# Kernel optimization log

Hardware: AMD Instinct MI355X
Metric: run time of the kernel (lower is better)

Reference implementation:

```python
import jax, jax.numpy as jnp
import numpy as np

B, T, D, H = 4, 2048, 1024, 16
Hd = D // H


def setup_inputs() -> dict:
    key = jax.random.key(0)
    ks = jax.random.split(key, 6)
    s = 1.0 / np.sqrt(D)
    return {
        "x": jax.random.normal(ks[0], (B, T, D), dtype=jnp.float32),
        "mask": jnp.zeros((B, T), dtype=bool),
        "Wq": jax.random.normal(ks[1], (D, D), dtype=jnp.float32) * s,
        "bq": jnp.zeros((D,), dtype=jnp.float32),
        "Wk": jax.random.normal(ks[2], (D, D), dtype=jnp.float32) * s,
        "bk": jnp.zeros((D,), dtype=jnp.float32),
        "Wv": jax.random.normal(ks[3], (D, D), dtype=jnp.float32) * s,
        "bv": jnp.zeros((D,), dtype=jnp.float32),
        "Wo": jax.random.normal(ks[4], (D, D), dtype=jnp.float32) * s,
        "bo": jnp.zeros((D,), dtype=jnp.float32),
    }


def reference(x, mask, Wq, bq, Wk, bk, Wv, bv, Wo, bo):
    b, t, d = x.shape
    # projections -> [B, T, H, Hd]
    Q = (x @ Wq + bq).reshape(b, t, H, Hd)
    K = (x @ Wk + bk).reshape(b, t, H, Hd)
    V = (x @ Wv + bv).reshape(b, t, H, Hd)
    scale = jnp.asarray(Hd, x.dtype) ** -0.5
    # full score matrix [B, H, Tq, Tk] (matches the naive torch impl)
    attn = jnp.einsum("bqhd,bkhd->bhqk", Q, K) * scale
    attn = jnp.where(mask[:, None, None, :], jnp.asarray(-1e9, attn.dtype), attn)
    attn = jax.nn.softmax(attn, axis=-1)
    out = jnp.einsum("bhqk,bkhd->bqhd", attn, V).reshape(b, t, d)
    return out @ Wo + bo
```

## Files before the change

kernel.cpp:

```cpp
#include <hip/hip_runtime.h>

using bf16 = __bf16;
typedef bf16 bf16x4 __attribute__((ext_vector_type(4)));
typedef bf16 bf16x8 __attribute__((ext_vector_type(8)));
typedef float f32x4 __attribute__((ext_vector_type(4)));
typedef float f32x8 __attribute__((ext_vector_type(8)));

#define MFMA16(a, b, c) __builtin_amdgcn_mfma_f32_16x16x32_bf16(a, b, c, 0, 0, 0)

constexpr int Bb = 4, Tt = 2048, Dd = 1024, Hh = 16, Hd = 64;
constexpr int Mrows = Bb * Tt;
constexpr float CEXP = 0.18033688011112042f;

__device__ __forceinline__ void gload_lds16(const bf16* g, bf16* lds_base) {
  __builtin_amdgcn_global_load_lds((const __attribute__((address_space(1))) void*)g,
                                   (__attribute__((address_space(3))) void*)lds_base,
                                   16, 0, 0);
}

__global__ void cast_f32_bf16_kernel(const float* __restrict__ in, bf16* __restrict__ out) {
  size_t i = ((size_t)blockIdx.x * 256 + threadIdx.x) * 8;
  f32x8 v = *(const f32x8*)(in + i);
  *(bf16x8*)(out + i) = __builtin_convertvector(v, bf16x8);
}

__global__ void transpose_cast_w4_kernel(const float* __restrict__ Wq, const float* __restrict__ Wk,
                                         const float* __restrict__ Wv, const float* __restrict__ Wo,
                                         bf16* __restrict__ Wt, bf16* __restrict__ Wot) {
  __shared__ alignas(16) float tile[64][68];
  const int tid = threadIdx.x;
  const int n0 = blockIdx.x * 64, k0 = blockIdx.y * 64, z = blockIdx.z;
  const float* W = (z == 0) ? Wq : (z == 1) ? Wk : (z == 2) ? Wv : Wo;
  bf16* dst = (z == 3) ? Wot : (Wt + (size_t)z * Dd * Dd);
  const float scale = (z == 0) ? CEXP : 1.0f;
#pragma unroll
  for (int it = 0; it < 4; ++it) {
    int chunk = tid + it * 256;
    int kr = chunk >> 4, c4 = chunk & 15;
    f32x4 v = *(const f32x4*)(W + (size_t)(k0 + kr) * Dd + n0 + c4 * 4);
    *(f32x4*)&tile[kr][c4 * 4] = v * scale;
  }
  __syncthreads();
#pragma unroll
  for (int it = 0; it < 2; ++it) {
    int chunk = tid + it * 256;
    int n = chunk & 63, k8 = chunk >> 6;
    bf16x8 o;
#pragma unroll
    for (int j = 0; j < 8; ++j) o[j] = (bf16)tile[k8 * 8 + j][n];
    *(bf16x8*)(dst + (size_t)(n0 + n) * Dd + k0 + k8 * 8) = o;
  }
}

__global__ void pack_bias_kernel(const float* __restrict__ bq, const float* __restrict__ bk,
                                 const float* __restrict__ bv, float* __restrict__ outb) {
  int i = blockIdx.x * 256 + threadIdx.x;
  float v = (i < 1024) ? bq[i] * CEXP : (i < 2048 ? bk[i - 1024] : bv[i - 2048]);
  outb[i] = v;
}

constexpr int QBM = 256, QBN = 256, QBK = 32, QNT = Dd / QBK;

#define VMW(n) asm volatile("s_waitcnt vmcnt(" #n ")" ::: "memory")

__global__ __launch_bounds__(512, 2)
void gemm_qkv_kernel(const bf16* __restrict__ A, const bf16* __restrict__ Bt,
                     const float* __restrict__ bias, bf16* __restrict__ QK,
                     bf16* __restrict__ Vt) {
  constexpr int KD = Dd;
  __shared__ alignas(16) bf16 As[4][QBM * QBK];
  __shared__ alignas(16) bf16 Bs[4][QBN * QBK];
  const int tid = threadIdx.x;
  const int lane = tid & 63, wave = tid >> 6;
  const int col = lane & 15, quad = lane >> 4;
  const int wr = wave >> 2, wc = wave & 3;
  const size_t m0 = (size_t)blockIdx.x * QBM, n0 = (size_t)blockIdx.y * QBN;

  const int u = (lane & 7) ^ (lane >> 3);
  const int srow = 2 * (lane >> 3) + (u >> 2);
  const int scol = (u & 3) * 8;
  const bf16* Abase = A + (m0 + srow) * (size_t)KD + scol;
  const bf16* Bbase = Bt + (n0 + srow) * (size_t)KD + scol;

  const int pswz = (((col & 1) << 2) | quad) ^ (col >> 1);
  const int afb = wr * 4096 + (col >> 1) * 64 + pswz * 8;
  const int bfb = wc * 2048 + (col >> 1) * 64 + pswz * 8;

  f32x4 acc[8][4];
#pragma unroll
  for (int i = 0; i < 8; ++i)
#pragma unroll
    for (int j = 0; j < 4; ++j)
#pragma unroll
      for (int r = 0; r < 4; ++r) acc[i][j][r] = 0.f;

#define QSTAGE_A(t, sl) do { \
    gload_lds16(Abase + (size_t)(t) * QBK + (size_t)(2 * wave + 0) * 16 * KD, &As[sl][(2 * wave + 0) * 512]); \
    gload_lds16(Abase + (size_t)(t) * QBK + (size_t)(2 * wave + 1) * 16 * KD, &As[sl][(2 * wave + 1) * 512]); \
  } while (0)
#define QSTAGE_B(t, sl) do { \
    gload_lds16(Bbase + (size_t)(t) * QBK + (size_t)(2 * wave + 0) * 16 * KD, &Bs[sl][(2 * wave + 0) * 512]); \
    gload_lds16(Bbase + (size_t)(t) * QBK + (size_t)(2 * wave + 1) * 16 * KD, &Bs[sl][(2 * wave + 1) * 512]); \
  } while (0)

#define QKV_TILE(sl, STAGE0, STAGE1, VM) do { \
    bf16x8 af[4], bfv[4]; \
    _Pragma("unroll") for (int j = 0; j < 4; ++j) bfv[j] = *(const bf16x8*)&Bs[sl][bfb + j * 512]; \
    _Pragma("unroll") for (int i = 0; i < 4; ++i) af[i] = *(const bf16x8*)&As[sl][afb + i * 512]; \
    STAGE0; \
    __builtin_amdgcn_s_barrier(); \
    asm volatile("s_waitcnt lgkmcnt(0)" ::: "memory"); \
    __builtin_amdgcn_s_setprio(1); \
    _Pragma("unroll") for (int i = 0; i < 4; ++i) \
      _Pragma("unroll") for (int j = 0; j < 4; ++j) acc[i][j] = MFMA16(af[i], bfv[j], acc[i][j]); \
    __builtin_amdgcn_s_setprio(0); \
    __builtin_amdgcn_s_barrier(); \
    _Pragma("unroll") for (int i = 0; i < 4; ++i) af[i] = *(const bf16x8*)&As[sl][afb + (4 + i) * 512]; \
    STAGE1; \
    __builtin_amdgcn_s_barrier(); \
    asm volatile("s_waitcnt lgkmcnt(0)" ::: "memory"); \
    __builtin_amdgcn_s_setprio(1); \
    _Pragma("unroll") for (int i = 0; i < 4; ++i) \
      _Pragma("unroll") for (int j = 0; j < 4; ++j) acc[4 + i][j] = MFMA16(af[i], bfv[j], acc[4 + i][j]); \
    __builtin_amdgcn_s_setprio(0); \
    VM; \
    __builtin_amdgcn_s_barrier(); \
  } while (0)

  QSTAGE_A(0, 0); QSTAGE_B(0, 0);
  QSTAGE_A(1, 1); QSTAGE_B(1, 1);
  QSTAGE_A(2, 2); QSTAGE_B(2, 2);
  VMW(8);
  __builtin_amdgcn_s_barrier();

#pragma unroll 1
  for (int t = 0; t < QNT - 4; t += 4) {
    QKV_TILE(0, QSTAGE_A(t + 3, 3), QSTAGE_B(t + 3, 3), VMW(8));
    QKV_TILE(1, QSTAGE_A(t + 4, 0), QSTAGE_B(t + 4, 0), VMW(8));
    QKV_TILE(2, QSTAGE_A(t + 5, 1), QSTAGE_B(t + 5, 1), VMW(8));
    QKV_TILE(3, QSTAGE_A(t + 6, 2), QSTAGE_B(t + 6, 2), VMW(8));
  }
  QKV_TILE(0, QSTAGE_A(31, 3), QSTAGE_B(31, 3), VMW(8));
  QKV_TILE(1, (void)0, (void)0, VMW(4));
  QKV_TILE(2, (void)0, (void)0, VMW(0));
  QKV_TILE(3, (void)0, (void)0, (void)0);

  if (n0 < 2048) {
#pragma unroll
    for (int i = 0; i < 8; ++i)
#pragma unroll
      for (int j = 0; j < 4; ++j) {
        size_t row = m0 + wr * 128 + i * 16 + quad * 4;
        size_t c = n0 + wc * 64 + j * 16 + col;
        float bv = bias[c];
#pragma unroll
        for (int r = 0; r < 4; ++r) QK[(row + r) * 2048 + c] = (bf16)(acc[i][j][r] + bv);
      }
  } else {
#pragma unroll
    for (int i = 0; i < 8; ++i)
#pragma unroll
      for (int j = 0; j < 4; ++j) {
        size_t row = m0 + wr * 128 + i * 16 + quad * 4;
        int c = (int)(n0 + wc * 64 + j * 16 + col);
        float bv = bias[c];
        int dall = c - 2048, hh = dall >> 6, dd = dall & 63;
        int bi = (int)(row >> 11), trow = (int)(row & 2047);
        bf16x4 pk;
#pragma unroll
        for (int r = 0; r < 4; ++r) pk[r] = (bf16)(acc[i][j][r] + bv);
        *(bf16x4*)&Vt[((size_t)(bi * Hh + hh) * Hd + dd) * Tt + trow] = pk;
      }
  }
#undef QKV_TILE
#undef QSTAGE_A
#undef QSTAGE_B
}

__global__ __launch_bounds__(256)
void gemm_bf16_kernel(const bf16* __restrict__ A, const bf16* __restrict__ Bt,
                      const float* __restrict__ bias, float* __restrict__ C,
                      int M, int N, int K) {
  __shared__ alignas(16) bf16 As[128 * 64];
  __shared__ alignas(16) bf16 Bs[128 * 64];
  const int tid = threadIdx.x;
  const int lane = tid & 63, wave = tid >> 6;
  const int col = lane & 15, quad = lane >> 4;
  const int wr = (wave >> 1) * 64, wc = (wave & 1) * 64;
  const size_t m0 = (size_t)blockIdx.x * 128, n0 = (size_t)blockIdx.y * 128;
  const int srow = lane >> 3, schunk = (lane & 7) * 8;

  f32x4 acc[4][4];
#pragma unroll
  for (int i = 0; i < 4; ++i)
#pragma unroll
    for (int j = 0; j < 4; ++j)
#pragma unroll
      for (int r = 0; r < 4; ++r) acc[i][j][r] = 0.f;

  for (int k0 = 0; k0 < K; k0 += 64) {
#pragma unroll
    for (int it = 0; it < 4; ++it) {
      int rbase = it * 32 + wave * 8;
      gload_lds16(A + (m0 + rbase + srow) * (size_t)K + k0 + schunk, &As[rbase * 64]);
      gload_lds16(Bt + (n0 + rbase + srow) * (size_t)K + k0 + schunk, &Bs[rbase * 64]);
    }
    __syncthreads();
#pragma unroll
    for (int kk = 0; kk < 2; ++kk) {
      bf16x8 af[4], bfr[4];
#pragma unroll
      for (int i = 0; i < 4; ++i) af[i] = *(const bf16x8*)&As[(wr + i * 16 + col) * 64 + kk * 32 + quad * 8];
#pragma unroll
      for (int j = 0; j < 4; ++j) bfr[j] = *(const bf16x8*)&Bs[(wc + j * 16 + col) * 64 + kk * 32 + quad * 8];
#pragma unroll
      for (int i = 0; i < 4; ++i)
#pragma unroll
        for (int j = 0; j < 4; ++j) acc[i][j] = MFMA16(af[i], bfr[j], acc[i][j]);
    }
    __syncthreads();
  }
#pragma unroll
  for (int i = 0; i < 4; ++i)
#pragma unroll
    for (int j = 0; j < 4; ++j) {
      size_t row = m0 + wr + i * 16 + quad * 4;
      size_t c = n0 + wc + j * 16 + col;
      float bv = bias[c];
#pragma unroll
      for (int r = 0; r < 4; ++r) C[(row + r) * (size_t)N + c] = acc[i][j][r] + bv;
    }
}

__global__ __launch_bounds__(256, 2)
void flash_attn_kernel(const bf16* __restrict__ qk, const bf16* __restrict__ vt,
                       const unsigned char* __restrict__ mask, bf16* __restrict__ ao) {
  __shared__ alignas(16) bf16 Ks[2][64 * 64];
  __shared__ alignas(16) bf16 Vs[2][64 * 64];

  const int tid = threadIdx.x;
  const int wave = tid >> 6, lane = tid & 63;
  const int col = lane & 15, quad = lane >> 4;
  const int id = blockIdx.x;
  const int hb = id & 63, qi = id >> 6;
  const int h = hb & 15, b = hb >> 4;
  const int qbase0 = qi * 128 + wave * 32;

  const bf16* Qp = qk + (size_t)(b * Tt) * 2048 + h * Hd;
  const bf16* Kp = Qp + 1024;
  const bf16* Vp = vt + ((size_t)(b * Hh + h) * Hd) * Tt;
  const unsigned char* mp = mask + b * Tt;

  unsigned long long anym;
  {
    const unsigned long long* mq = (const unsigned long long*)mp;
    unsigned long long acc = 0;
#pragma unroll
    for (int j = 0; j < 4; ++j) acc |= mq[lane * 4 + j];
    anym = __ballot(acc != 0ull);
  }

  bf16x8 qf[2][2];
#pragma unroll
  for (int t = 0; t < 2; ++t)
#pragma unroll
    for (int kk = 0; kk < 2; ++kk)
      qf[t][kk] = *(const bf16x8*)(Qp + (size_t)(qbase0 + t * 16 + col) * 2048 + kk * 32 + quad * 8);

  const int u = (lane & 7) ^ (lane >> 3);
  const int g0 = 2 * wave, g1 = 2 * wave + 1;
  const bf16* Ksrc0 = Kp + (size_t)(g0 * 8 + (lane >> 3)) * 2048 + u * 8;
  const bf16* Ksrc1 = Kp + (size_t)(g1 * 8 + (lane >> 3)) * 2048 + u * 8;
  const bf16* Vsrc0 = Vp + (size_t)(g0 * 8 + (lane >> 3)) * 2048 + u * 8;
  const bf16* Vsrc1 = Vp + (size_t)(g1 * 8 + (lane >> 3)) * 2048 + u * 8;

  gload_lds16(Ksrc0, &Ks[0][g0 * 512]);
  gload_lds16(Ksrc1, &Ks[0][g1 * 512]);
  gload_lds16(Vsrc0, &Vs[0][g0 * 512]);
  gload_lds16(Vsrc1, &Vs[0][g1 * 512]);
  __syncthreads();

  f32x4 oacc[2][4];
  f32x4 lones[2];
#pragma unroll
  for (int t = 0; t < 2; ++t) {
#pragma unroll
    for (int r = 0; r < 4; ++r) lones[t][r] = 0.f;
#pragma unroll
    for (int n = 0; n < 4; ++n)
#pragma unroll
      for (int r = 0; r < 4; ++r) oacc[t][n][r] = 0.f;
  }
  const f32x4 zero4 = {0.f, 0.f, 0.f, 0.f};
  bf16x8 onev;
#pragma unroll
  for (int j = 0; j < 8; ++j) onev[j] = (bf16)1.0f;

  const int fslot0 = ((0 * 4 + quad) ^ (col & 7)) * 8;
  const int fslot1 = ((1 * 4 + quad) ^ (col & 7)) * 8;
  const int voff = (quad & 1) * 4;

  for (int i = 0; i < 32; ++i) {
    const int cur = i & 1, nxt = cur ^ 1;
    const int kb = i * 64;

    if (i < 31) {
      gload_lds16(Ksrc0 + (size_t)(kb + 64) * 2048, &Ks[nxt][g0 * 512]);
      gload_lds16(Ksrc1 + (size_t)(kb + 64) * 2048, &Ks[nxt][g1 * 512]);
      gload_lds16(Vsrc0 + (kb + 64), &Vs[nxt][g0 * 512]);
      gload_lds16(Vsrc1 + (kb + 64), &Vs[nxt][g1 * 512]);
    }

    bf16x8 kf[4][2], vfs[4][2];
#pragma unroll
    for (int kt = 0; kt < 4; ++kt) {
      kf[kt][0] = *(const bf16x8*)&Ks[cur][(kt * 16 + col) * 64 + fslot0];
      kf[kt][1] = *(const bf16x8*)&Ks[cur][(kt * 16 + col) * 64 + fslot1];
    }
#pragma unroll
    for (int n = 0; n < 4; ++n) {
      const int row = (n * 16 + col) * 64;
      const int rx = col & 7;
#pragma unroll
      for (int kk = 0; kk < 2; ++kk) {
        bf16x4 lo = *(const bf16x4*)&Vs[cur][row + ((kk * 4 + 0 + (quad >> 1)) ^ rx) * 8 + voff];
        bf16x4 hi = *(const bf16x4*)&Vs[cur][row + ((kk * 4 + 2 + (quad >> 1)) ^ rx) * 8 + voff];
        vfs[n][kk] = __builtin_shufflevector(lo, hi, 0, 1, 2, 3, 4, 5, 6, 7);
      }
    }

#pragma unroll
    for (int t = 0; t < 2; ++t) {
      f32x4 s[4];
#pragma unroll
      for (int kt = 0; kt < 4; ++kt) s[kt] = MFMA16(kf[kt][0], qf[t][0], zero4);
#pragma unroll
      for (int kt = 0; kt < 4; ++kt) s[kt] = MFMA16(kf[kt][1], qf[t][1], s[kt]);

      if ((anym >> (2 * i)) & 3ull) {
#pragma unroll
        for (int kt = 0; kt < 4; ++kt)
#pragma unroll
          for (int r = 0; r < 4; ++r)
            if (mp[kb + kt * 16 + quad * 4 + r] != 0) s[kt][r] = -1e9f;
      }

      f32x4 e[4];
#pragma unroll
      for (int kt = 0; kt < 4; ++kt)
#pragma unroll
        for (int r = 0; r < 4; ++r) e[kt][r] = __builtin_amdgcn_exp2f(s[kt][r]);
      bf16x4 c0 = __builtin_convertvector(e[0], bf16x4);
      bf16x4 c1 = __builtin_convertvector(e[1], bf16x4);
      bf16x4 c2 = __builtin_convertvector(e[2], bf16x4);
      bf16x4 c3 = __builtin_convertvector(e[3], bf16x4);
      bf16x8 pf0 = __builtin_shufflevector(c0, c1, 0, 1, 2, 3, 4, 5, 6, 7);
      bf16x8 pf1 = __builtin_shufflevector(c2, c3, 0, 1, 2, 3, 4, 5, 6, 7);
#pragma unroll
      for (int n = 0; n < 4; ++n) {
        oacc[t][n] = MFMA16(pf0, vfs[n][0], oacc[t][n]);
        oacc[t][n] = MFMA16(pf1, vfs[n][1], oacc[t][n]);
      }
      lones[t] = MFMA16(pf0, onev, lones[t]);
      lones[t] = MFMA16(pf1, onev, lones[t]);
    }

    __syncthreads();
  }

#pragma unroll
  for (int t = 0; t < 2; ++t) {
    f32x4 rl;
#pragma unroll
    for (int r = 0; r < 4; ++r) rl[r] = __builtin_amdgcn_rcpf(lones[t][r]);
#pragma unroll
    for (int n = 0; n < 4; ++n)
#pragma unroll
      for (int r = 0; r < 4; ++r) {
        size_t q = (size_t)b * Tt + qbase0 + t * 16 + quad * 4 + r;
        ao[q * Dd + h * Hd + n * 16 + col] = (bf16)(oacc[t][n][r] * rl[r]);
      }
  }
}

extern "C" void kernel_launch(void* const* d_in, const int* in_sizes, int n_in,
                              void* d_out, int out_size, void* d_ws, size_t ws_size,
                              hipStream_t stream) {
  const float* x = (const float*)d_in[0];
  const unsigned char* mask = (const unsigned char*)d_in[1];
  const float* Wq = (const float*)d_in[2];
  const float* bq = (const float*)d_in[3];
  const float* Wk = (const float*)d_in[4];
  const float* bk = (const float*)d_in[5];
  const float* Wv = (const float*)d_in[6];
  const float* bv = (const float*)d_in[7];
  const float* Wo = (const float*)d_in[8];
  const float* bo = (const float*)d_in[9];
  float* out = (float*)d_out;

  char* ws = (char*)d_ws;
  size_t off = 0;
  auto alloc = [&](size_t bytes) {
    char* p = ws + off;
    off += (bytes + 255) & ~(size_t)255;
    return p;
  };
  bf16* xb  = (bf16*)alloc((size_t)Mrows * Dd * 2);
  bf16* Wt  = (bf16*)alloc((size_t)3 * Dd * Dd * 2);
  bf16* Wot = (bf16*)alloc((size_t)Dd * Dd * 2);
  bf16* QK  = (bf16*)alloc((size_t)Mrows * 2048 * 2);
  bf16* Vt  = (bf16*)alloc((size_t)Bb * Hh * Hd * Tt * 2);
  float* bqkv = (float*)alloc((size_t)3 * Dd * 4);

  cast_f32_bf16_kernel<<<Mrows * Dd / (256 * 8), 256, 0, stream>>>(x, xb);
  transpose_cast_w4_kernel<<<dim3(16, 16, 4), 256, 0, stream>>>(Wq, Wk, Wv, Wo, Wt, Wot);
  pack_bias_kernel<<<12, 256, 0, stream>>>(bq, bk, bv, bqkv);

  gemm_qkv_kernel<<<dim3(Mrows / QBM, 3 * Dd / QBN), 512, 0, stream>>>(
      xb, Wt, bqkv, QK, Vt);

  bf16* AO = xb;
  flash_attn_kernel<<<dim3(1024), 256, 0, stream>>>(QK, Vt, mask, AO);
  gemm_bf16_kernel<<<dim3(Mrows / 128, Dd / 128), 256, 0, stream>>>(
      AO, Wot, bo, out, Mrows, Dd, Dd);
}
```

Before: 288.9 us.

## Shrink QKV GEMM tile to 128x256 with 3-stage pipeline; add MFMA priority in attention

```diff
diff --git a/kernel.cpp b/kernel.cpp
--- a/kernel.cpp
+++ b/kernel.cpp
@@ -59,7 +59,7 @@
   outb[i] = v;
 }
 
-constexpr int QBM = 256, QBN = 256, QBK = 32, QNT = Dd / QBK;
+constexpr int QBM = 128, QBN = 256, QBK = 32, QNT = Dd / QBK;
 
 #define VMW(n) asm volatile("s_waitcnt vmcnt(" #n ")" ::: "memory")
 
@@ -68,8 +68,8 @@
                      const float* __restrict__ bias, bf16* __restrict__ QK,
                      bf16* __restrict__ Vt) {
   constexpr int KD = Dd;
-  __shared__ alignas(16) bf16 As[4][QBM * QBK];
-  __shared__ alignas(16) bf16 Bs[4][QBN * QBK];
+  __shared__ alignas(16) bf16 As[3][QBM * QBK];
+  __shared__ alignas(16) bf16 Bs[3][QBN * QBK];
   const int tid = threadIdx.x;
   const int lane = tid & 63, wave = tid >> 6;
   const int col = lane & 15, quad = lane >> 4;
@@ -83,74 +83,57 @@
   const bf16* Bbase = Bt + (n0 + srow) * (size_t)KD + scol;
 
   const int pswz = (((col & 1) << 2) | quad) ^ (col >> 1);
-  const int afb = wr * 4096 + (col >> 1) * 64 + pswz * 8;
+  const int afb = wr * 2048 + (col >> 1) * 64 + pswz * 8;
   const int bfb = wc * 2048 + (col >> 1) * 64 + pswz * 8;
 
-  f32x4 acc[8][4];
-#pragma unroll
-  for (int i = 0; i < 8; ++i)
+  f32x4 acc[4][4];
+#pragma unroll
+  for (int i = 0; i < 4; ++i)
 #pragma unroll
     for (int j = 0; j < 4; ++j)
 #pragma unroll
       for (int r = 0; r < 4; ++r) acc[i][j][r] = 0.f;
 
-#define QSTAGE_A(t, sl) do { \
-    gload_lds16(Abase + (size_t)(t) * QBK + (size_t)(2 * wave + 0) * 16 * KD, &As[sl][(2 * wave + 0) * 512]); \
-    gload_lds16(Abase + (size_t)(t) * QBK + (size_t)(2 * wave + 1) * 16 * KD, &As[sl][(2 * wave + 1) * 512]); \
-  } while (0)
-#define QSTAGE_B(t, sl) do { \
-    gload_lds16(Bbase + (size_t)(t) * QBK + (size_t)(2 * wave + 0) * 16 * KD, &Bs[sl][(2 * wave + 0) * 512]); \
+#define QSTAGE(t, sl) do { \
+    gload_lds16(Abase + (size_t)(t) * QBK + (size_t)(wave * 16) * KD, &As[sl][wave * 512]); \
+    gload_lds16(Bbase + (size_t)(t) * QBK + (size_t)(2 * wave) * 16 * KD, &Bs[sl][(2 * wave) * 512]); \
     gload_lds16(Bbase + (size_t)(t) * QBK + (size_t)(2 * wave + 1) * 16 * KD, &Bs[sl][(2 * wave + 1) * 512]); \
   } while (0)
 
-#define QKV_TILE(sl, STAGE0, STAGE1, VM) do { \
+#define QKV_TILE(cur, DOSTAGE, VM) do { \
     bf16x8 af[4], bfv[4]; \
-    _Pragma("unroll") for (int j = 0; j < 4; ++j) bfv[j] = *(const bf16x8*)&Bs[sl][bfb + j * 512]; \
-    _Pragma("unroll") for (int i = 0; i < 4; ++i) af[i] = *(const bf16x8*)&As[sl][afb + i * 512]; \
-    STAGE0; \
-    __builtin_amdgcn_s_barrier(); \
+    _Pragma("unroll") for (int j = 0; j < 4; ++j) bfv[j] = *(const bf16x8*)&Bs[cur][bfb + j * 512]; \
+    _Pragma("unroll") for (int i = 0; i < 4; ++i) af[i] = *(const bf16x8*)&As[cur][afb + i * 512]; \
+    DOSTAGE; \
     asm volatile("s_waitcnt lgkmcnt(0)" ::: "memory"); \
     __builtin_amdgcn_s_setprio(1); \
     _Pragma("unroll") for (int i = 0; i < 4; ++i) \
       _Pragma("unroll") for (int j = 0; j < 4; ++j) acc[i][j] = MFMA16(af[i], bfv[j], acc[i][j]); \
     __builtin_amdgcn_s_setprio(0); \
-    __builtin_amdgcn_s_barrier(); \
-    _Pragma("unroll") for (int i = 0; i < 4; ++i) af[i] = *(const bf16x8*)&As[sl][afb + (4 + i) * 512]; \
-    STAGE1; \
-    __builtin_amdgcn_s_barrier(); \
-    asm volatile("s_waitcnt lgkmcnt(0)" ::: "memory"); \
-    __builtin_amdgcn_s_setprio(1); \
-    _Pragma("unroll") for (int i = 0; i < 4; ++i) \
-      _Pragma("unroll") for (int j = 0; j < 4; ++j) acc[4 + i][j] = MFMA16(af[i], bfv[j], acc[4 + i][j]); \
-    __builtin_amdgcn_s_setprio(0); \
     VM; \
     __builtin_amdgcn_s_barrier(); \
   } while (0)
 
-  QSTAGE_A(0, 0); QSTAGE_B(0, 0);
-  QSTAGE_A(1, 1); QSTAGE_B(1, 1);
-  QSTAGE_A(2, 2); QSTAGE_B(2, 2);
-  VMW(8);
+  QSTAGE(0, 0);
+  QSTAGE(1, 1);
+  VMW(3);
   __builtin_amdgcn_s_barrier();
 
 #pragma unroll 1
-  for (int t = 0; t < QNT - 4; t += 4) {
-    QKV_TILE(0, QSTAGE_A(t + 3, 3), QSTAGE_B(t + 3, 3), VMW(8));
-    QKV_TILE(1, QSTAGE_A(t + 4, 0), QSTAGE_B(t + 4, 0), VMW(8));
-    QKV_TILE(2, QSTAGE_A(t + 5, 1), QSTAGE_B(t + 5, 1), VMW(8));
-    QKV_TILE(3, QSTAGE_A(t + 6, 2), QSTAGE_B(t + 6, 2), VMW(8));
-  }
-  QKV_TILE(0, QSTAGE_A(31, 3), QSTAGE_B(31, 3), VMW(8));
-  QKV_TILE(1, (void)0, (void)0, VMW(4));
-  QKV_TILE(2, (void)0, (void)0, VMW(0));
-  QKV_TILE(3, (void)0, (void)0, (void)0);
+  for (int t = 0; t < QNT - 2; t += 3) {
+    QKV_TILE(0, QSTAGE(t + 2, 2), VMW(3));
+    QKV_TILE(1, QSTAGE(t + 3, 0), VMW(3));
+    QKV_TILE(2, QSTAGE(t + 4, 1), VMW(3));
+  }
+  QKV_TILE(0, (void)0, VMW(0));
+  QKV_TILE(1, (void)0, (void)0);
 
   if (n0 < 2048) {
 #pragma unroll
-    for (int i = 0; i < 8; ++i)
+    for (int i = 0; i < 4; ++i)
 #pragma unroll
       for (int j = 0; j < 4; ++j) {
-        size_t row = m0 + wr * 128 + i * 16 + quad * 4;
+        size_t row = m0 + wr * 64 + i * 16 + quad * 4;
         size_t c = n0 + wc * 64 + j * 16 + col;
         float bv = bias[c];
 #pragma unroll
@@ -158,10 +141,10 @@
       }
   } else {
 #pragma unroll
-    for (int i = 0; i < 8; ++i)
+    for (int i = 0; i < 4; ++i)
 #pragma unroll
       for (int j = 0; j < 4; ++j) {
-        size_t row = m0 + wr * 128 + i * 16 + quad * 4;
+        size_t row = m0 + wr * 64 + i * 16 + quad * 4;
         int c = (int)(n0 + wc * 64 + j * 16 + col);
         float bv = bias[c];
         int dall = c - 2048, hh = dall >> 6, dd = dall & 63;
@@ -173,8 +156,7 @@
       }
   }
 #undef QKV_TILE
-#undef QSTAGE_A
-#undef QSTAGE_B
+#undef QSTAGE
 }
 
 __global__ __launch_bounds__(256)
@@ -332,10 +314,12 @@
 #pragma unroll
     for (int t = 0; t < 2; ++t) {
       f32x4 s[4];
+      __builtin_amdgcn_s_setprio(1);
 #pragma unroll
       for (int kt = 0; kt < 4; ++kt) s[kt] = MFMA16(kf[kt][0], qf[t][0], zero4);
 #pragma unroll
       for (int kt = 0; kt < 4; ++kt) s[kt] = MFMA16(kf[kt][1], qf[t][1], s[kt]);
+      __builtin_amdgcn_s_setprio(0);
 
       if ((anym >> (2 * i)) & 3ull) {
 #pragma unroll
@@ -356,6 +340,7 @@
       bf16x4 c3 = __builtin_convertvector(e[3], bf16x4);
       bf16x8 pf0 = __builtin_shufflevector(c0, c1, 0, 1, 2, 3, 4, 5, 6, 7);
       bf16x8 pf1 = __builtin_shufflevector(c2, c3, 0, 1, 2, 3, 4, 5, 6, 7);
+      __builtin_amdgcn_s_setprio(1);
 #pragma unroll
       for (int n = 0; n < 4; ++n) {
         oacc[t][n] = MFMA16(pf0, vfs[n][0], oacc[t][n]);
@@ -363,6 +348,7 @@
       }
       lones[t] = MFMA16(pf0, onev, lones[t]);
       lones[t] = MFMA16(pf1, onev, lones[t]);
+      __builtin_amdgcn_s_setprio(0);
     }
 
     __syncthreads();
```

Result: no change. 294.3 us (+1.9%).
